# Performance work log

Hardware: AMD Instinct MI355X
Metric: run time of the kernel (lower is better)

The kernel has to match this reference:

```python
import jax, jax.numpy as jnp
import numpy as np

SHIFT = 1e-09  # input_shift


def _patches(v, kh, kw):
    # v: (B, C, H, W) -> (B, C, kh*kw, Ho, Wo), VALID padding, stride 1
    B, C, H, W = v.shape
    Ho, Wo = H - kh + 1, W - kw + 1
    cols = [v[:, :, i:i + Ho, j:j + Wo] for i in range(kh) for j in range(kw)]
    return jnp.stack(cols, axis=2)


def setup_inputs() -> dict:
    key = jax.random.key(0)
    kx, k1k, k2k, kb = jax.random.split(key, 4)
    B, C, H, W = 32, 64, 64, 64
    kh, kw, F = 3, 3, 128
    x = jax.random.normal(kx, (B, C, H, W), dtype=jnp.float32)
    # log-domain kernels (learned params of the two Add modules)
    k1 = jax.random.normal(k1k, (kh, kw, C, F), dtype=jnp.float32) * 0.1
    k2 = jax.random.normal(k2k, (kh, kw, C, F), dtype=jnp.float32) * 0.1
    bias = jnp.zeros((F,), dtype=jnp.float32)
    return {"x": x, "k1": k1, "k2": k2, "bias": bias}


def reference(x, k1, k2, bias):
    kh, kw, C, F = k1.shape
    # Ln: log of ReLU'd patches (positive and negative parts of x)
    ep_pos = jnp.exp(jnp.log(jax.nn.relu(_patches(x, kh, kw)) + SHIFT))   # (B,C,kh*kw,Ho,Wo)
    ep_neg = jnp.exp(jnp.log(jax.nn.relu(_patches(-x, kh, kw)) + SHIFT))
    # Add + Exp + patch reduction: sum_p exp(ln_patch + k) == einsum(exp(ln_patch), exp(k))
    ek1 = jnp.exp(k1).reshape(kh * kw, C, F)
    ek2 = jnp.exp(k2).reshape(kh * kw, C, F)
    y11 = jnp.einsum('bckhw,kcf->bfhw', ep_pos, ek1)
    y12 = jnp.einsum('bckhw,kcf->bfhw', ep_pos, ek2)
    y21 = jnp.einsum('bckhw,kcf->bfhw', ep_neg, ek1)
    y22 = jnp.einsum('bckhw,kcf->bfhw', ep_neg, ek2)
    return y11 - y12 - y21 + y22 + bias[None, :, None, None]
```

## Files before the change

kernel.cpp:

```cpp
#include <hip/hip_runtime.h>
#include <hip/hip_bf16.h>

typedef __attribute__((ext_vector_type(4))) float f32x4;
typedef __attribute__((ext_vector_type(8))) short bf16x8;

static __device__ __forceinline__ unsigned int f2bf(float f) {
    unsigned int u = __float_as_uint(f);
    return (u + 0x7FFFu + ((u >> 16) & 1u)) >> 16;
}

__global__ __launch_bounds__(256) void wprep_kernel(const float* __restrict__ k1,
                                                    const float* __restrict__ k2,
                                                    unsigned short* __restrict__ wq) {
    int idx = blockIdx.x * 256 + threadIdx.x;
    if (idx >= 73728) return;
    int f  = idx & 127;
    int ch = (idx >> 7) & 31;
    int kh = (idx >> 12) & 1;
    int p  = idx >> 13;
    int src = (p * 64 + kh * 32 + ch) * 128 + f;
    float v = expf(k1[src]) - expf(k2[src]);
    wq[((p * 2 + kh) * 128 + f) * 32 + ch] = (unsigned short)f2bf(v);
}

__global__ __launch_bounds__(256, 3) void conv_kernel(const float* __restrict__ x,
                                                      const unsigned short* __restrict__ wq,
                                                      const float* __restrict__ bias,
                                                      float* __restrict__ out) {
    __shared__ unsigned short xs[4 * 64 * 64];

    int bid0 = blockIdx.x;
    int bid  = (bid0 & 7) * 124 + (bid0 >> 3);
    int b    = bid / 31;
    int tile = bid - b * 31;
    int oh0  = tile * 2;

    int tid  = threadIdx.x;
    int lane = tid & 63;
    int wid  = tid >> 6;
    int wr   = wid >> 1;
    int wc   = wid & 1;
    int lr   = lane & 15;
    int hi   = lane >> 4;

    const float* xb = x + b * (64 * 4096);

    {
        int col = tid & 63;
#pragma unroll
        for (int j = 0; j < 8; ++j) {
            int u   = wid + j * 4;
            int row = u >> 3;
            int cg  = u & 7;
            float v[8];
#pragma unroll
            for (int e = 0; e < 8; ++e)
                v[e] = xb[(cg * 8 + e) * 4096 + (oh0 + row) * 64 + col];
            uint4 pk;
            pk.x = f2bf(v[0]) | (f2bf(v[1]) << 16);
            pk.y = f2bf(v[2]) | (f2bf(v[3]) << 16);
            pk.z = f2bf(v[4]) | (f2bf(v[5]) << 16);
            pk.w = f2bf(v[6]) | (f2bf(v[7]) << 16);
            *(uint4*)(&xs[((row * 64 + col) << 6) + ((cg * 8) ^ ((col & 7) << 3))]) = pk;
        }
    }

    const bf16x8* wg = (const bf16x8*)wq;
    int fb0 = wc * 64 + lr;
    bf16x8 wfrag[2][8];
#pragma unroll
    for (int kh = 0; kh < 2; ++kh)
#pragma unroll
        for (int ni = 0; ni < 4; ++ni)
            wfrag[0][kh * 4 + ni] = wg[((kh) * 128 + fb0 + ni * 16) * 4 + hi];

    f32x4 acc[4][4];
#pragma unroll
    for (int ni = 0; ni < 4; ++ni)
#pragma unroll
        for (int mi = 0; mi < 4; ++mi) acc[ni][mi] = (f32x4){0.f, 0.f, 0.f, 0.f};

    __syncthreads();

#pragma unroll
    for (int p = 0; p < 9; ++p) {
        const int cur = p & 1, nxt = cur ^ 1;
        if (p < 8) {
#pragma unroll
            for (int kh = 0; kh < 2; ++kh)
#pragma unroll
                for (int ni = 0; ni < 4; ++ni)
                    wfrag[nxt][kh * 4 + ni] = wg[(((p + 1) * 2 + kh) * 128 + fb0 + ni * 16) * 4 + hi];
        }
        const int ki = p / 3, kj = p % 3;
#pragma unroll
        for (int kb = 0; kb < 2; ++kb) {
            int c0 = kb * 32 + hi * 8;
            bf16x8 af[4];
#pragma unroll
            for (int mi = 0; mi < 4; ++mi) {
                int col  = mi * 16 + lr + kj;
                int colc = col > 63 ? 63 : col;
                af[mi] = *(const bf16x8*)(&xs[(((wr + ki) * 64 + colc) << 6) + (c0 ^ ((colc & 7) << 3))]);
            }
#pragma unroll
            for (int ni = 0; ni < 4; ++ni)
#pragma unroll
                for (int mi = 0; mi < 4; ++mi)
                    acc[ni][mi] = __builtin_amdgcn_mfma_f32_16x16x32_bf16(
                        wfrag[cur][kb * 4 + ni], af[mi], acc[ni][mi], 0, 0, 0);
        }
    }

    int oh = oh0 + wr;
    float* ob = out + b * (128 * 62 * 62);
#pragma unroll
    for (int ni = 0; ni < 4; ++ni) {
        int fb = wc * 64 + ni * 16 + (hi << 2);
        f32x4 bv4 = *(const f32x4*)(bias + fb);
#pragma unroll
        for (int t = 0; t < 4; ++t) {
            float* orow = ob + ((fb + t) * 62 + oh) * 62;
#pragma unroll
            for (int mi = 0; mi < 4; ++mi) {
                int ow = mi * 16 + lr;
                if (ow < 62) orow[ow] = acc[ni][mi][t] + bv4[t];
            }
        }
    }
}

extern "C" void kernel_launch(void* const* d_in, const int* in_sizes, int n_in,
                              void* d_out, int out_size, void* d_ws, size_t ws_size,
                              hipStream_t stream) {
    const float* x    = (const float*)d_in[0];
    const float* k1   = (const float*)d_in[1];
    const float* k2   = (const float*)d_in[2];
    const float* bias = (const float*)d_in[3];
    float* out = (float*)d_out;

    unsigned short* wq = (unsigned short*)d_ws;

    hipLaunchKernelGGL(wprep_kernel, dim3(288), dim3(256), 0, stream, k1, k2, wq);
    hipLaunchKernelGGL(conv_kernel, dim3(992), dim3(256), 0, stream, x, wq, bias, out);
}
```

Baseline: 133.0 us.

## Pre-convert input to swizzled bf16 NHWC and stage via direct global-to-LDS loads

A new prep kernel transposes x from NCHW fp32 into a channel-last bf16 buffer that already uses the LDS swizzle. The conv kernel then fills shared memory with global_load_lds 16-byte copies instead of strided fp32 loads followed by conversion. The goal is to remove uncoalesced strided reads and repeated conversion work, since each input row is loaded by several overlapping tiles. In exchange it adds a kernel launch and a full extra write and read of the bf16 input, and lowers the launch-bounds occupancy hint from 3 to 2.

```diff
diff --git a/kernel.cpp b/kernel.cpp
--- a/kernel.cpp
+++ b/kernel.cpp
@@ -7,6 +7,12 @@
 static __device__ __forceinline__ unsigned int f2bf(float f) {
     unsigned int u = __float_as_uint(f);
     return (u + 0x7FFFu + ((u >> 16) & 1u)) >> 16;
+}
+
+static __device__ __forceinline__ void gload_lds16(const void* g, void* l) {
+    __builtin_amdgcn_global_load_lds(
+        (const __attribute__((address_space(1))) unsigned int*)g,
+        (__attribute__((address_space(3))) unsigned int*)l, 16, 0, 0);
 }
 
 __global__ __launch_bounds__(256) void wprep_kernel(const float* __restrict__ k1,
@@ -23,7 +29,39 @@
     wq[((p * 2 + kh) * 128 + f) * 32 + ch] = (unsigned short)f2bf(v);
 }
 
-__global__ __launch_bounds__(256, 3) void conv_kernel(const float* __restrict__ x,
+__global__ __launch_bounds__(256) void xprep_kernel(const float* __restrict__ x,
+                                                    unsigned short* __restrict__ xsw) {
+    __shared__ float t[64][65];
+    int b = blockIdx.x >> 6;
+    int h = blockIdx.x & 63;
+    const float* xb = x + b * 262144 + h * 64;
+    int tid = threadIdx.x;
+    int col4 = (tid & 15) * 4;
+    int c0   = tid >> 4;
+#pragma unroll
+    for (int i = 0; i < 4; ++i) {
+        int c = c0 + i * 16;
+        f32x4 v = *(const f32x4*)(xb + c * 4096 + col4);
+        t[c][col4 + 0] = v[0]; t[c][col4 + 1] = v[1];
+        t[c][col4 + 2] = v[2]; t[c][col4 + 3] = v[3];
+    }
+    __syncthreads();
+    unsigned short* orow = xsw + ((b * 64 + h) * 64) * 64;
+#pragma unroll
+    for (int i = 0; i < 2; ++i) {
+        int j   = tid + i * 256;
+        int col = j >> 3;
+        int cb  = ((j & 7) ^ (col & 7)) * 8;
+        uint4 pk;
+        pk.x = f2bf(t[cb + 0][col]) | (f2bf(t[cb + 1][col]) << 16);
+        pk.y = f2bf(t[cb + 2][col]) | (f2bf(t[cb + 3][col]) << 16);
+        pk.z = f2bf(t[cb + 4][col]) | (f2bf(t[cb + 5][col]) << 16);
+        pk.w = f2bf(t[cb + 6][col]) | (f2bf(t[cb + 7][col]) << 16);
+        *(uint4*)(orow + j * 8) = pk;
+    }
+}
+
+__global__ __launch_bounds__(256, 2) void conv_kernel(const unsigned short* __restrict__ xsw,
                                                       const unsigned short* __restrict__ wq,
                                                       const float* __restrict__ bias,
                                                       float* __restrict__ out) {
@@ -43,25 +81,13 @@
     int lr   = lane & 15;
     int hi   = lane >> 4;
 
-    const float* xb = x + b * (64 * 4096);
-
     {
-        int col = tid & 63;
+        const char* src = (const char*)(xsw + ((b * 64 + oh0) * 64) * 64);
+        char* dst = (char*)xs;
 #pragma unroll
-        for (int j = 0; j < 8; ++j) {
-            int u   = wid + j * 4;
-            int row = u >> 3;
-            int cg  = u & 7;
-            float v[8];
-#pragma unroll
-            for (int e = 0; e < 8; ++e)
-                v[e] = xb[(cg * 8 + e) * 4096 + (oh0 + row) * 64 + col];
-            uint4 pk;
-            pk.x = f2bf(v[0]) | (f2bf(v[1]) << 16);
-            pk.y = f2bf(v[2]) | (f2bf(v[3]) << 16);
-            pk.z = f2bf(v[4]) | (f2bf(v[5]) << 16);
-            pk.w = f2bf(v[6]) | (f2bf(v[7]) << 16);
-            *(uint4*)(&xs[((row * 64 + col) << 6) + ((cg * 8) ^ ((col & 7) << 3))]) = pk;
+        for (int i = 0; i < 8; ++i) {
+            int chunk = (i * 4 + wid) * 1024;
+            gload_lds16(src + chunk + lane * 16, dst + chunk);
         }
     }
 
@@ -72,7 +98,7 @@
     for (int kh = 0; kh < 2; ++kh)
 #pragma unroll
         for (int ni = 0; ni < 4; ++ni)
-            wfrag[0][kh * 4 + ni] = wg[((kh) * 128 + fb0 + ni * 16) * 4 + hi];
+            wfrag[0][kh * 4 + ni] = wg[(kh * 128 + fb0 + ni * 16) * 4 + hi];
 
     f32x4 acc[4][4];
 #pragma unroll
@@ -139,8 +165,10 @@
     const float* bias = (const float*)d_in[3];
     float* out = (float*)d_out;
 
-    unsigned short* wq = (unsigned short*)d_ws;
+    unsigned short* wq  = (unsigned short*)d_ws;
+    unsigned short* xsw = (unsigned short*)d_ws + 73728;
 
     hipLaunchKernelGGL(wprep_kernel, dim3(288), dim3(256), 0, stream, k1, k2, wq);
-    hipLaunchKernelGGL(conv_kernel, dim3(992), dim3(256), 0, stream, x, wq, bias, out);
+    hipLaunchKernelGGL(xprep_kernel, dim3(2048), dim3(256), 0, stream, x, xsw);
+    hipLaunchKernelGGL(conv_kernel, dim3(992), dim3(256), 0, stream, x  == nullptr ? xsw : xsw, wq, bias, out);
 }
```

New measurement: 136.3 us. +2.5%, slower.
